# Kernel optimization log

Hardware: AMD Instinct MI355X
Metric: run time of the kernel (lower is better)

The kernel has to match this reference:

```python
import jax, jax.numpy as jnp
import numpy as np

B, S, D, H, R = 4, 2048, 4096, 4096, 16
Q_SCALE = K_SCALE = V_SCALE = 1.0


def setup_inputs() -> dict:
    key = jax.random.key(0)
    ks = jax.random.split(key, 10)
    sd = 0.02
    return {
        "x": jax.random.normal(ks[0], (B, S, D), dtype=jnp.float32),
        "q_weight": jax.random.normal(ks[1], (H, D), dtype=jnp.float32) * sd,
        "k_weight": jax.random.normal(ks[2], (H, D), dtype=jnp.float32) * sd,
        "v_weight": jax.random.normal(ks[3], (H, D), dtype=jnp.float32) * sd,
        "q_A": jax.random.normal(ks[4], (R, D), dtype=jnp.float32) * sd,
        "q_B": jax.random.normal(ks[5], (H, R), dtype=jnp.float32) * sd,
        "k_A": jax.random.normal(ks[6], (R, D), dtype=jnp.float32) * sd,
        "k_B": jax.random.normal(ks[7], (H, R), dtype=jnp.float32) * sd,
        "v_A": jax.random.normal(ks[8], (R, D), dtype=jnp.float32) * sd,
        "v_B": jax.random.normal(ks[9], (H, R), dtype=jnp.float32) * sd,
    }


def _matmul_lora(x, W, A, Bm, s):
    # x: [B,S,D]; W: [H,D] (torch Linear layout, applied as x @ W.T)
    # LoRA: A [R,D], B [H,R] -> out += (x @ A.T) @ (s * B.T)
    main = jnp.einsum("bsd,hd->bsh", x, W)
    lora = jnp.einsum("bsr,hr->bsh", jnp.einsum("bsd,rd->bsr", x, A), s * Bm)
    return main + lora


def reference(x, q_weight, k_weight, v_weight, q_A, q_B, k_A, k_B, v_A, v_B):
    Q = _matmul_lora(x, q_weight, q_A, q_B, Q_SCALE)
    K = _matmul_lora(x, k_weight, k_A, k_B, K_SCALE)
    V = _matmul_lora(x, v_weight, v_A, v_B, V_SCALE)
    return (Q, K, V)
```

## Files before the change

### kernel.cpp

```cpp
#include <hip/hip_runtime.h>


typedef __bf16 bf16x8 __attribute__((ext_vector_type(8)));
typedef float f32x4 __attribute__((ext_vector_type(4)));

#define GLL16(g, l)                                                        \
  __builtin_amdgcn_global_load_lds(                                        \
      (const __attribute__((address_space(1))) unsigned int*)(g),          \
      (__attribute__((address_space(3))) unsigned int*)(l), 16, 0, 0)

#define BAR()                                                              \
  {                                                                        \
    __builtin_amdgcn_sched_barrier(0);                                     \
    __builtin_amdgcn_s_barrier();                                          \
  }
#define WLG(n) asm volatile("s_waitcnt lgkmcnt(" #n ")" ::: "memory")
#define WVM(n) asm volatile("s_waitcnt vmcnt(" #n ")" ::: "memory")

#define LDV(p) (*reinterpret_cast<const bf16x8*>(p))

#define RDA(dst, base, M0)                                                 \
  _Pragma("unroll") for (int mm = 0; mm < 4; ++mm) {                       \
    dst[0][mm] = LDV((base) + ((M0) + mm) * 1024 + swk0);                  \
    dst[1][mm] = LDV((base) + ((M0) + mm) * 1024 + swk1);                  \
  }
#define RDB(dst, base, N0)                                                 \
  _Pragma("unroll") for (int nn = 0; nn < 2; ++nn) {                       \
    dst[0][nn] = LDV((base) + ((N0) + nn) * 1024 + swk0);                  \
    dst[1][nn] = LDV((base) + ((N0) + nn) * 1024 + swk1);                  \
  }

#define MFQ(AQ, BQ, MB, NB)                                                \
  {                                                                        \
    __builtin_amdgcn_s_setprio(1);                                         \
    _Pragma("unroll") for (int ks = 0; ks < 2; ++ks)                       \
        _Pragma("unroll") for (int mm = 0; mm < 4; ++mm)                   \
            _Pragma("unroll") for (int nn = 0; nn < 2; ++nn)               \
                acc[(MB) + mm][(NB) + nn] =                                \
                    __builtin_amdgcn_mfma_f32_16x16x32_bf16(               \
                        AQ[ks][mm], BQ[ks][nn], acc[(MB) + mm][(NB) + nn], \
                        0, 0, 0);                                          \
    __builtin_amdgcn_s_setprio(0);                                         \
  }

#define STG_A(db, h, ko)                                                   \
  {                                                                        \
    GLL16(sa + (size_t)((h)*128) * 4096 + (ko),                            \
          (char*)smem + (db)*65536 + (h)*16384 + tid * 16);                \
    GLL16(sa + (size_t)((h)*128 + 64) * 4096 + (ko),                       \
          (char*)smem + (db)*65536 + (h)*16384 + 8192 + tid * 16);         \
  }
#define STG_B(db, h, ko)                                                   \
  {                                                                        \
    GLL16(sb + (size_t)((h)*128) * 4096 + (ko),                            \
          (char*)smem + (db)*65536 + 32768 + (h)*16384 + tid * 16);        \
    GLL16(sb + (size_t)((h)*128 + 64) * 4096 + (ko),                       \
          (char*)smem + (db)*65536 + 32768 + (h)*16384 + 8192 + tid * 16); \
  }

__device__ __forceinline__ unsigned int f2b(float f) {
  unsigned int u = __builtin_bit_cast(unsigned int, f);
  u += 0x7FFFu + ((u >> 16) & 1u);
  return u >> 16;
}

__global__ void prep_kernel(const float* __restrict__ x,
                            const float* __restrict__ w0,
                            const float* __restrict__ w1,
                            const float* __restrict__ w2,
                            const float* __restrict__ a0,
                            const float* __restrict__ b0,
                            const float* __restrict__ a1,
                            const float* __restrict__ b1,
                            const float* __restrict__ a2,
                            const float* __restrict__ b2,
                            unsigned short* __restrict__ xb,
                            unsigned short* __restrict__ wb) {
  __shared__ float As[16][512];
  const int bid = blockIdx.x;
  const int tid = threadIdx.x;
  if (bid < 8192) {
    long base = ((long)bid * 256 + tid) * 2;
    const float4* xp = reinterpret_cast<const float4*>(x) + base * 2;
#pragma unroll
    for (int j = 0; j < 2; ++j) {
      float4 v0 = xp[2 * j];
      float4 v1 = xp[2 * j + 1];
      uint4 o;
      o.x = f2b(v0.x) | (f2b(v0.y) << 16);
      o.y = f2b(v0.z) | (f2b(v0.w) << 16);
      o.z = f2b(v1.x) | (f2b(v1.y) << 16);
      o.w = f2b(v1.z) | (f2b(v1.w) << 16);
      reinterpret_cast<uint4*>(xb)[base + j] = o;
    }
  } else {
    const int fb = bid - 8192;
    const int proj = fb >> 10;
    const int rem = fb & 1023;
    const int h0 = (rem >> 3) * 32;
    const int d0b = (rem & 7) * 512;
    const float* W = (proj == 0) ? w0 : ((proj == 1) ? w1 : w2);
    const float* Amat = (proj == 0) ? a0 : ((proj == 1) ? a1 : a2);
    const float* Bmat = (proj == 0) ? b0 : ((proj == 1) ? b1 : b2);
    unsigned short* Wo = wb + (size_t)proj * 16777216UL;

#pragma unroll
    for (int j = 0; j < 8; ++j) {
      int idx4 = tid + j * 256;
      int row = idx4 >> 7;
      int col4 = idx4 & 127;
      float4 v = *reinterpret_cast<const float4*>(
          Amat + (size_t)row * 4096 + d0b + col4 * 4);
      *reinterpret_cast<float4*>(&As[row][col4 * 4]) = v;
    }
    __syncthreads();

    const int hl = tid >> 3;
    const int dl = (tid & 7) * 8;
    const int h = h0 + hl;
    float bv[16];
#pragma unroll
    for (int r = 0; r < 16; ++r) bv[r] = Bmat[h * 16 + r];

#pragma unroll
    for (int c = 0; c < 8; ++c) {
      const int d = dl + c * 64;
      const float4* wp =
          reinterpret_cast<const float4*>(W + (size_t)h * 4096 + d0b + d);
      float4 w0v = wp[0], w1v = wp[1];
      float acc[8] = {w0v.x, w0v.y, w0v.z, w0v.w,
                      w1v.x, w1v.y, w1v.z, w1v.w};
#pragma unroll
      for (int r = 0; r < 16; ++r) {
        const float4 A0 = *reinterpret_cast<const float4*>(&As[r][d]);
        const float4 A1 = *reinterpret_cast<const float4*>(&As[r][d + 4]);
        acc[0] += bv[r] * A0.x; acc[1] += bv[r] * A0.y;
        acc[2] += bv[r] * A0.z; acc[3] += bv[r] * A0.w;
        acc[4] += bv[r] * A1.x; acc[5] += bv[r] * A1.y;
        acc[6] += bv[r] * A1.z; acc[7] += bv[r] * A1.w;
      }
      uint4 o;
      o.x = f2b(acc[0]) | (f2b(acc[1]) << 16);
      o.y = f2b(acc[2]) | (f2b(acc[3]) << 16);
      o.z = f2b(acc[4]) | (f2b(acc[5]) << 16);
      o.w = f2b(acc[6]) | (f2b(acc[7]) << 16);
      *reinterpret_cast<uint4*>(Wo + (size_t)h * 4096 + d0b + d) = o;
    }
  }
}

__global__ __launch_bounds__(512, 2) void gemm_kernel(
    const unsigned short* __restrict__ Xb,
    const unsigned short* __restrict__ Wb, float* __restrict__ out) {
  __shared__ unsigned short smem[65536];

  const int tid = threadIdx.x;
  const int lane = tid & 63;
  const int wid = tid >> 6;
  const int wm = wid >> 2;
  const int wn = wid & 3;

  int bid = blockIdx.x;
  int swz = (bid & 7) * 192 + (bid >> 3);
  int p = swz >> 9;
  int r = swz & 511;
  int brow = r >> 4;
  int bcol = r & 15;

  const unsigned short* GA = Xb + (size_t)brow * 256 * 4096;
  const unsigned short* GB =
      Wb + (size_t)p * 16777216UL + (size_t)bcol * 256 * 4096;

  const int srow = tid >> 3;
  const int sslot = (tid & 7) ^ (srow & 7);
  const unsigned short* sa = GA + (size_t)srow * 4096 + sslot * 8;
  const unsigned short* sb = GB + (size_t)srow * 4096 + sslot * 8;

  const int lrow = lane & 15;
  const int g = lane >> 4;
  const int swk0 = (g ^ (lane & 7)) * 8;
  const int swk1 = ((4 + g) ^ (lane & 7)) * 8;
  const __bf16* sm = (const __bf16*)smem;
  const __bf16* arA0 = sm + wm * 8192 + lrow * 64;
  const __bf16* arB0 =
      sm + 16384 + (wn >> 1) * 8192 + ((wn & 1) * 64 + lrow) * 64;
  const __bf16* arA1 = arA0 + 32768;
  const __bf16* arB1 = arB0 + 32768;

  f32x4 acc[8][4];
#pragma unroll
  for (int m = 0; m < 8; ++m)
#pragma unroll
    for (int n = 0; n < 4; ++n) acc[m][n] = {0.f, 0.f, 0.f, 0.f};

  STG_B(0, 0, 0); STG_B(0, 1, 0); STG_A(0, 0, 0); STG_A(0, 1, 0);
  WVM(4);
  STG_B(1, 0, 64); STG_B(1, 1, 64); STG_A(1, 0, 64);
  WVM(6);
  BAR();

  bf16x8 aLo[2][4], aHi[2][4], bLo[2][2], bHi[2][2];

  for (int i = 0; i < 32; ++i) {
    const bool st = (i < 31);
    const size_t koD1 = (size_t)(2 * i + 1) * 64;
    const size_t koN0 = (size_t)(2 * i + 2) * 64;
    const size_t koN1 = (size_t)(2 * i + 3) * 64;

    RDA(aLo, arA0, 0);
    RDB(bLo, arB0, 0);
    STG_A(1, 1, koD1);
    WLG(8);
    BAR();
    WLG(0);
    MFQ(aLo, bLo, 0, 0);
    BAR();
    RDB(bHi, arB0, 2);
    if (st) STG_B(0, 0, koN0);
    BAR();
    WLG(0);
    MFQ(aLo, bHi, 0, 2);
    BAR();
    RDA(aHi, arA0, 4);
    if (st) STG_B(0, 1, koN0);
    BAR();
    WLG(0);
    MFQ(aHi, bHi, 4, 2);
    BAR();
    if (st) {
      STG_A(0, 0, koN0);
      WVM(6);
    } else {
      WVM(0);
    }
    BAR();
    MFQ(aHi, bLo, 4, 0);
    BAR();

    RDA(aLo, arA1, 0);
    RDB(bLo, arB1, 0);
    if (st) STG_A(0, 1, koN0);
    WLG(8);
    BAR();
    WLG(0);
    MFQ(aLo, bLo, 0, 0);
    BAR();
    RDB(bHi, arB1, 2);
    if (st) STG_B(1, 0, koN1);
    BAR();
    WLG(0);
    MFQ(aLo, bHi, 0, 2);
    BAR();
    RDA(aHi, arA1, 4);
    if (st) STG_B(1, 1, koN1);
    BAR();
    WLG(0);
    MFQ(aHi, bHi, 4, 2);
    BAR();
    if (st) {
      STG_A(1, 0, koN1);
      WVM(6);
    }
    BAR();
    MFQ(aHi, bLo, 4, 0);
    BAR();
  }

  float* Cp = out + (size_t)p * 33554432UL +
              ((size_t)(brow * 256 + wm * 128 + g * 4)) * 4096 +
              (bcol * 256 + wn * 64 + lrow);
#pragma unroll
  for (int m = 0; m < 8; ++m)
#pragma unroll
    for (int q = 0; q < 4; ++q) {
      float* rp = Cp + (size_t)(m * 16 + q) * 4096;
#pragma unroll
      for (int n = 0; n < 4; ++n) rp[n * 16] = acc[m][n][q];
    }
}

extern "C" void kernel_launch(void* const* d_in, const int* in_sizes, int n_in,
                              void* d_out, int out_size, void* d_ws,
                              size_t ws_size, hipStream_t stream) {
  const float* x = (const float*)d_in[0];
  const float* wq = (const float*)d_in[1];
  const float* wk = (const float*)d_in[2];
  const float* wv = (const float*)d_in[3];
  const float* qa = (const float*)d_in[4];
  const float* qb = (const float*)d_in[5];
  const float* ka = (const float*)d_in[6];
  const float* kb = (const float*)d_in[7];
  const float* va = (const float*)d_in[8];
  const float* vb = (const float*)d_in[9];

  unsigned short* xb = (unsigned short*)d_ws;
  unsigned short* wb = xb + 8192UL * 4096UL;

  prep_kernel<<<11264, 256, 0, stream>>>(x, wq, wk, wv, qa, qb, ka, kb, va,
                                         vb, xb, wb);
  gemm_kernel<<<1536, 512, 0, stream>>>(xb, wb, (float*)d_out);
}
```

Measured before the change: 783.4 us.

## Overlap LDS fragment reads with MFMAs and halve barriers in GEMM main loop

Restructures the double-buffered GEMM main loop so the next LDS fragment reads are issued right after each MFMA block instead of behind their own barrier. This removes about half the workgroup barriers per iteration, and the loop is software-pipelined so the first fragment reads of the next stage are issued at the end of the previous iteration. Global-to-LDS stages are grouped in pairs with adjusted vmcnt waits, and sched_barriers are added around barriers and waits so the compiler cannot reorder across them. It depends on the buffer-reuse ordering remaining race-free with fewer barriers.

After: 762.1 us. 1.03x faster.

```diff
diff --git a/kernel.cpp b/kernel.cpp
--- a/kernel.cpp
+++ b/kernel.cpp
@@ -13,8 +13,13 @@
   {                                                                        \
     __builtin_amdgcn_sched_barrier(0);                                     \
     __builtin_amdgcn_s_barrier();                                          \
-  }
-#define WLG(n) asm volatile("s_waitcnt lgkmcnt(" #n ")" ::: "memory")
+    __builtin_amdgcn_sched_barrier(0);                                     \
+  }
+#define WLGS(n)                                                            \
+  {                                                                        \
+    asm volatile("s_waitcnt lgkmcnt(" #n ")" ::: "memory");                \
+    __builtin_amdgcn_sched_barrier(0);                                     \
+  }
 #define WVM(n) asm volatile("s_waitcnt vmcnt(" #n ")" ::: "memory")
 
 #define LDV(p) (*reinterpret_cast<const bf16x8*>(p))
@@ -193,77 +198,73 @@
 #pragma unroll
     for (int n = 0; n < 4; ++n) acc[m][n] = {0.f, 0.f, 0.f, 0.f};
 
+  bf16x8 aLo[2][4], aHi[2][4], bLo[2][2], bHi[2][2];
+
   STG_B(0, 0, 0); STG_B(0, 1, 0); STG_A(0, 0, 0); STG_A(0, 1, 0);
+  STG_B(1, 0, 64); STG_B(1, 1, 64);
   WVM(4);
-  STG_B(1, 0, 64); STG_B(1, 1, 64); STG_A(1, 0, 64);
-  WVM(6);
   BAR();
-
-  bf16x8 aLo[2][4], aHi[2][4], bLo[2][2], bHi[2][2];
+  RDA(aLo, arA0, 0);
+  RDB(bLo, arB0, 0);
+  STG_A(1, 0, 64); STG_A(1, 1, 64);
 
   for (int i = 0; i < 32; ++i) {
     const bool st = (i < 31);
-    const size_t koD1 = (size_t)(2 * i + 1) * 64;
     const size_t koN0 = (size_t)(2 * i + 2) * 64;
     const size_t koN1 = (size_t)(2 * i + 3) * 64;
 
-    RDA(aLo, arA0, 0);
-    RDB(bLo, arB0, 0);
-    STG_A(1, 1, koD1);
-    WLG(8);
-    BAR();
-    WLG(0);
+    BAR();
+    WLGS(0);
     MFQ(aLo, bLo, 0, 0);
-    BAR();
     RDB(bHi, arB0, 2);
-    if (st) STG_B(0, 0, koN0);
-    BAR();
-    WLG(0);
+    BAR();
+    WLGS(0);
     MFQ(aLo, bHi, 0, 2);
-    BAR();
     RDA(aHi, arA0, 4);
-    if (st) STG_B(0, 1, koN0);
-    BAR();
-    WLG(0);
+    BAR();
+    WLGS(0);
     MFQ(aHi, bHi, 4, 2);
-    BAR();
+    if (st) {
+      STG_B(0, 0, koN0);
+      STG_B(0, 1, koN0);
+      WVM(4);
+    } else {
+      WVM(0);
+    }
+    BAR();
+    WLGS(0);
+    MFQ(aHi, bLo, 4, 0);
+    RDA(aLo, arA1, 0);
+    RDB(bLo, arB1, 0);
     if (st) {
       STG_A(0, 0, koN0);
-      WVM(6);
-    } else {
-      WVM(0);
-    }
-    BAR();
+      STG_A(0, 1, koN0);
+    }
+    BAR();
+    WLGS(0);
+    MFQ(aLo, bLo, 0, 0);
+    RDB(bHi, arB1, 2);
+    BAR();
+    WLGS(0);
+    MFQ(aLo, bHi, 0, 2);
+    RDA(aHi, arA1, 4);
+    BAR();
+    WLGS(0);
+    MFQ(aHi, bHi, 4, 2);
+    if (st) {
+      STG_B(1, 0, koN1);
+      STG_B(1, 1, koN1);
+      WVM(4);
+    }
+    BAR();
+    WLGS(0);
     MFQ(aHi, bLo, 4, 0);
-    BAR();
-
-    RDA(aLo, arA1, 0);
-    RDB(bLo, arB1, 0);
-    if (st) STG_A(0, 1, koN0);
-    WLG(8);
-    BAR();
-    WLG(0);
-    MFQ(aLo, bLo, 0, 0);
-    BAR();
-    RDB(bHi, arB1, 2);
-    if (st) STG_B(1, 0, koN1);
-    BAR();
-    WLG(0);
-    MFQ(aLo, bHi, 0, 2);
-    BAR();
-    RDA(aHi, arA1, 4);
-    if (st) STG_B(1, 1, koN1);
-    BAR();
-    WLG(0);
-    MFQ(aHi, bHi, 4, 2);
-    BAR();
     if (st) {
+      RDA(aLo, arA0, 0);
+      RDB(bLo, arB0, 0);
       STG_A(1, 0, koN1);
-      WVM(6);
-    }
-    BAR();
-    MFQ(aHi, bLo, 4, 0);
-    BAR();
+      STG_A(1, 1, koN1);
+    }
   }
 
   float* Cp = out + (size_t)p * 33554432UL +
```
